# Kernel optimization log

Measured on AMD Instinct MI355X. Metric: run time of the kernel, lower is better.

Reference implementation:

```python
import jax, jax.numpy as jnp
import numpy as np

PAD = 2
STRIDE = 1

def _cayley(sig):
    # Geometric-product Cayley table G[i, j, k]: e_i * e_j = G[i, j, i^j] e_{i^j}
    # Blades indexed by bitmask over generators; sig = metric signature (+1/-1 per generator).
    n = len(sig)
    dim = 1 << n
    G = np.zeros((dim, dim, dim), dtype=np.float32)
    for a in range(dim):
        for b in range(dim):
            s = 0
            aa = a >> 1
            while aa:
                s += bin(aa & b).count('1')
                aa >>= 1
            sign = -1.0 if (s & 1) else 1.0
            common = a & b
            for i, m in enumerate(sig):
                if (common >> i) & 1:
                    sign *= m
            G[a, b, a ^ b] = sign
    return G


def setup_inputs() -> dict:
    key = jax.random.key(0)
    k1, k2, k3 = jax.random.split(key, 3)
    B, C, O, BD, L, K = 8, 64, 64, 8, 4096, 5
    x = jax.random.normal(k1, (B, C, BD, L), dtype=jnp.float32)
    bound = 1.0 / np.sqrt(C * BD * K)  # kaiming-style uniform bound
    W = jax.random.uniform(k2, (K, C, O, BD), minval=-bound, maxval=bound, dtype=jnp.float32)
    b = jax.random.uniform(k3, (1, O, BD, 1), minval=-bound, maxval=bound, dtype=jnp.float32)
    G = jnp.asarray(_cayley((1.0, 1.0, 1.0)))  # Cl(3,0), basis_dim = 8
    return {"x": x, "W": W, "b": b, "G": G}


def reference(x, W, b, G):
    # Original: pad length dim, unfold windows, then
    # result[b,o,k,w] = sum_{i,j,c,v} G[i,j,k] * W[v,c,o,i] * x_pad[b,c,j,w+v], plus bias.
    # Equivalent efficient form: pre-contract G with W into a conv kernel over
    # fused (channel, basis) axes and run a standard 1D convolution.
    K = W.shape[0]
    B, C, J, L = x.shape
    O = W.shape[2]
    Kb = G.shape[2]
    xp = jnp.pad(x, ((0, 0), (0, 0), (0, 0), (PAD, PAD)))  # padding_mode='zeros'
    # T[o,k,c,j,v] = sum_i G[i,j,k] W[v,c,o,i]  (tiny tensor: O*Kb x C*J x K)
    kern = jnp.einsum('ijk,vcoi->okcjv', G, W).reshape(O * Kb, C * J, K)
    xin = xp.reshape(B, C * J, L + 2 * PAD)
    out = jax.lax.conv_general_dilated(
        xin, kern, window_strides=(STRIDE,), padding='VALID',
        dimension_numbers=('NCH', 'OIH', 'NCH'))
    # out channels are (o major, k minor) per the reshape above
    return out.reshape(B, O, Kb, out.shape[-1]) + b
```

## Files before the change

### kernel.cpp

```cpp
#include <hip/hip_runtime.h>


#define C_    64
#define L_    4096
#define PAD_  2
#define OKch  512
#define KD_   2560

#define BM    128
#define BN    128
#define BKCJ  64
#define NCJB  8
#define NV    5
#define TILE  8192
#define ASTR  72
#define WIN   132

typedef __bf16 bf16x8 __attribute__((ext_vector_type(8)));
typedef float floatx4 __attribute__((ext_vector_type(4)));

__device__ __forceinline__ unsigned short f2bf(float f) {
    unsigned int u = __float_as_uint(f);
    u += 0x7FFFu + ((u >> 16) & 1u);
    return (unsigned short)(u >> 16);
}

#define WAIT_LGKM_0() asm volatile("s_waitcnt lgkmcnt(0)" ::: "memory")

__device__ __forceinline__ void barrier_raw() {
    asm volatile("" ::: "memory");
    __builtin_amdgcn_sched_barrier(0);
    __builtin_amdgcn_s_barrier();
    __builtin_amdgcn_sched_barrier(0);
    asm volatile("" ::: "memory");
}

__global__ __launch_bounds__(256) void build_kern(
    const float* __restrict__ W, const float* __restrict__ G,
    unsigned short* __restrict__ kernT)
{
    const int idx  = blockIdx.x * 256 + threadIdx.x;
    const int lrow = idx & 15;
    const int quad = (idx >> 4) & 3;
    const int f    = (idx >> 6) & 15;
    const int mq   = f >> 1;
    const int kk2  = f & 1;
    const int t    = idx >> 10;
    const int v    = t % 5;
    const int tc   = t / 5;
    const int cjb  = tc & 7;
    const int y    = tc >> 3;
    const int m    = (mq << 4) | lrow;
    const int ok   = (y << 7) | m;
    const int o    = ok >> 3;
    const int kb   = ok & 7;
    const int c    = (cjb << 3) | (kk2 << 2) | quad;

    const float* Wp = W + (((v * C_ + c) * 64 + o) << 3);
    const float4 w0 = *(const float4*)Wp;
    const float4 w1 = *(const float4*)(Wp + 4);
    const float w[8] = {w0.x, w0.y, w0.z, w0.w, w1.x, w1.y, w1.z, w1.w};

    unsigned int pk[4];
    #pragma unroll
    for (int j = 0; j < 8; j++) {
        float s = 0.f;
        #pragma unroll
        for (int i = 0; i < 8; i++)
            s += G[i * 64 + j * 8 + kb] * w[i];
        const unsigned short h = f2bf(s);
        if (j & 1) pk[j >> 1] |= (unsigned int)h << 16;
        else       pk[j >> 1]  = h;
    }
    uint4 uu; uu.x = pk[0]; uu.y = pk[1]; uu.z = pk[2]; uu.w = pk[3];
    *reinterpret_cast<uint4*>(
        &kernT[((size_t)t << 13) + (f << 9) + (quad << 7) + (lrow << 3)]) = uu;
}

__device__ __forceinline__ void b_issue(const float* xb, int cj0, int w0,
                                        float br[5][8]) {
    const int tid = threadIdx.x;
    #pragma unroll
    for (int u = 0; u < 5; u++) {
        int idx; bool act;
        if (u < 4) { idx = u * 256 + tid; act = true; }
        else { act = ((tid & 7) == 0);
               idx = 1024 + ((tid >> 6) << 3) + ((tid >> 3) & 7); }
        if (act) {
            const int kgrp = idx / WIN;
            const int nn   = idx - kgrp * WIN;
            int ws = w0 - PAD_ + nn;
            ws = ws < 0 ? 0 : (ws > (L_ - 1) ? (L_ - 1) : ws);
            const float* xp = xb + ((size_t)(cj0 + (kgrp << 3)) << 12) + (size_t)ws;
            #pragma unroll
            for (int r = 0; r < 8; r++)
                br[u][r] = xp[(size_t)r << 12];
        }
    }
}

__device__ __forceinline__ void b_store(unsigned short* BsP, const float br[5][8],
                                        int w0) {
    const int tid = threadIdx.x;
    #pragma unroll
    for (int u = 0; u < 5; u++) {
        int idx; bool act;
        if (u < 4) { idx = u * 256 + tid; act = true; }
        else { act = ((tid & 7) == 0);
               idx = 1024 + ((tid >> 6) << 3) + ((tid >> 3) & 7); }
        if (act) {
            const int kgrp = idx / WIN;
            const int nn   = idx - kgrp * WIN;
            const bool inb = (unsigned)(w0 - PAD_ + nn) < (unsigned)L_;
            unsigned int pk[4];
            #pragma unroll
            for (int r = 0; r < 8; r++) {
                const unsigned short h = f2bf(inb ? br[u][r] : 0.0f);
                if (r & 1) pk[r >> 1] |= (unsigned int)h << 16;
                else       pk[r >> 1]  = h;
            }
            uint4 uu; uu.x = pk[0]; uu.y = pk[1]; uu.z = pk[2]; uu.w = pk[3];
            *reinterpret_cast<uint4*>(&BsP[nn * ASTR + (kgrp << 3)]) = uu;
        }
    }
}

__device__ __forceinline__ void a_load(const unsigned short* t, int wb,
                                       bf16x8 r[8]) {
    #pragma unroll
    for (int f = 0; f < 8; f++)
        r[f] = *reinterpret_cast<const bf16x8*>(t + (f << 9) + wb);
}

__device__ __forceinline__ void compute_phase(
    const bf16x8 a[8], const unsigned short* BsP,
    int wn, int lrow, int quad, int v, floatx4 acc[4][4])
{
    #pragma unroll
    for (int kk2 = 0; kk2 < 2; kk2++) {
        bf16x8 bfr[4];
        #pragma unroll
        for (int nt = 0; nt < 4; nt++)
            bfr[nt] = *reinterpret_cast<const bf16x8*>(
                &BsP[(wn + (nt << 4) + lrow + v) * ASTR + (kk2 << 5) + (quad << 3)]);
        __builtin_amdgcn_s_setprio(1);
        #pragma unroll
        for (int mt = 0; mt < 4; mt++)
            #pragma unroll
            for (int nt = 0; nt < 4; nt++)
                acc[mt][nt] = __builtin_amdgcn_mfma_f32_16x16x32_bf16(
                    a[mt * 2 + kk2], bfr[nt], acc[mt][nt], 0, 0, 0);
        __builtin_amdgcn_s_setprio(0);
    }
}

__global__ __launch_bounds__(256, 2) void gpconv_mfma(
    const float* __restrict__ x, const unsigned short* __restrict__ kernT,
    const float* __restrict__ bias, float* __restrict__ out)
{
    __shared__ unsigned short Bs[WIN * ASTR];

    const int tid  = threadIdx.x;
    const int lane = tid & 63;
    const int wave = tid >> 6;
    const int lrow = lane & 15;
    const int quad = lane >> 4;
    const int wm = (wave >> 1) << 6;
    const int wn = (wave & 1) << 6;

    const int bid = blockIdx.x;
    const int y   = (bid >> 3) & 3;
    const int xw  = ((bid >> 5) << 3) + (bid & 7);
    const int b   = xw >> 5;
    const int w0  = (xw & 31) * BN;
    const int mBase = y * BM;
    const float* xb = x + (size_t)b * (size_t)(512 * L_);
    const unsigned short* ky = kernT + (size_t)(y * NCJB) * NV * TILE;

    const int wb = wm * 64 + lane * 8;

    floatx4 acc[4][4];
    {
        const floatx4 z = {0.f, 0.f, 0.f, 0.f};
        #pragma unroll
        for (int i2 = 0; i2 < 4; i2++)
            #pragma unroll
            for (int j2 = 0; j2 < 4; j2++) acc[i2][j2] = z;
    }

    bf16x8 aX[8], aY[8];
    float br[5][8];

    b_issue(xb, 0, w0, br);
    a_load(ky, wb, aX);
    b_store(Bs, br, w0);
    WAIT_LGKM_0();
    barrier_raw();

#define PHASE(CUR, NXT, CJB, V, DO_PRE, DO_BI, DO_ST)                        \
    {                                                                        \
        if (DO_PRE) a_load(ky + (size_t)((CJB) * 5 + (V) + 1) * TILE, wb, NXT); \
        if (DO_BI)  b_issue(xb, ((CJB) + 1) * BKCJ, w0, br);                 \
        compute_phase(CUR, Bs, wn, lrow, quad, (V), acc);                    \
        if (DO_ST) {                                                         \
            barrier_raw();                  \
            b_store(Bs, br, w0);       \
            WAIT_LGKM_0();                                                   \
            barrier_raw();                           \
        }                                                                    \
    }

    for (int cp = 0; cp < 3; cp++) {
        const int c0 = cp * 2, c1 = c0 + 1;
        PHASE(aX, aY, c0, 0, 1, 0, 0);
        PHASE(aY, aX, c0, 1, 1, 0, 0);
        PHASE(aX, aY, c0, 2, 1, 0, 0);
        PHASE(aY, aX, c0, 3, 1, 1, 0);
        PHASE(aX, aY, c0, 4, 1, 0, 1);
        PHASE(aY, aX, c1, 0, 1, 0, 0);
        PHASE(aX, aY, c1, 1, 1, 0, 0);
        PHASE(aY, aX, c1, 2, 1, 0, 0);
        PHASE(aX, aY, c1, 3, 1, 1, 0);
        PHASE(aY, aX, c1, 4, 1, 0, 1);
    }
    PHASE(aX, aY, 6, 0, 1, 0, 0);
    PHASE(aY, aX, 6, 1, 1, 0, 0);
    PHASE(aX, aY, 6, 2, 1, 0, 0);
    PHASE(aY, aX, 6, 3, 1, 1, 0);
    PHASE(aX, aY, 6, 4, 1, 0, 1);
    PHASE(aY, aX, 7, 0, 1, 0, 0);
    PHASE(aX, aY, 7, 1, 1, 0, 0);
    PHASE(aY, aX, 7, 2, 1, 0, 0);
    PHASE(aX, aY, 7, 3, 1, 0, 0);
    PHASE(aY, aX, 7, 4, 0, 0, 0);
#undef PHASE

    #pragma unroll
    for (int mt = 0; mt < 4; mt++) {
        #pragma unroll
        for (int e = 0; e < 4; e++) {
            const int okc = mBase + wm + (mt << 4) + (quad << 2) + e;
            const float bv = bias[okc];
            float* orow = out + ((size_t)b * OKch + (size_t)okc) * L_ + w0;
            #pragma unroll
            for (int nt = 0; nt < 4; nt++) {
                const int n = wn + (nt << 4) + lrow;
                orow[n] = acc[mt][nt][e] + bv;
            }
        }
    }
}

extern "C" void kernel_launch(void* const* d_in, const int* in_sizes, int n_in,
                              void* d_out, int out_size, void* d_ws, size_t ws_size,
                              hipStream_t stream) {
    const float* x    = (const float*)d_in[0];
    const float* W    = (const float*)d_in[1];
    const float* bias = (const float*)d_in[2];
    const float* G    = (const float*)d_in[3];
    unsigned short* kernT = (unsigned short*)d_ws;
    float* out = (float*)d_out;

    build_kern<<<dim3(640), 256, 0, stream>>>(W, G, kernT);
    gpconv_mfma<<<dim3(1024), 256, 0, stream>>>(x, kernT, bias, out);
}
```

Baseline: 184.9 us.

## Double-buffer x tile in LDS with XOR swizzle and split staged loads

```diff
diff --git a/kernel.cpp b/kernel.cpp
--- a/kernel.cpp
+++ b/kernel.cpp
@@ -13,8 +13,8 @@
 #define NCJB  8
 #define NV    5
 #define TILE  8192
-#define ASTR  72
 #define WIN   132
+#define BSZ   (WIN * 64)
 
 typedef __bf16 bf16x8 __attribute__((ext_vector_type(8)));
 typedef float floatx4 __attribute__((ext_vector_type(4)));
@@ -77,51 +77,73 @@
         &kernT[((size_t)t << 13) + (f << 9) + (quad << 7) + (lrow << 3)]) = uu;
 }
 
-__device__ __forceinline__ void b_issue(const float* xb, int cj0, int w0,
-                                        float br[5][8]) {
-    const int tid = threadIdx.x;
-    #pragma unroll
-    for (int u = 0; u < 5; u++) {
-        int idx; bool act;
-        if (u < 4) { idx = u * 256 + tid; act = true; }
-        else { act = ((tid & 7) == 0);
-               idx = 1024 + ((tid >> 6) << 3) + ((tid >> 3) & 7); }
-        if (act) {
-            const int kgrp = idx / WIN;
-            const int nn   = idx - kgrp * WIN;
-            int ws = w0 - PAD_ + nn;
-            ws = ws < 0 ? 0 : (ws > (L_ - 1) ? (L_ - 1) : ws);
-            const float* xp = xb + ((size_t)(cj0 + (kgrp << 3)) << 12) + (size_t)ws;
-            #pragma unroll
-            for (int r = 0; r < 8; r++)
-                br[u][r] = xp[(size_t)r << 12];
-        }
-    }
-}
-
-__device__ __forceinline__ void b_store(unsigned short* BsP, const float br[5][8],
+__device__ __forceinline__ void bi_half(const float* xb, int cj0, int w0,
+                                        int base, float br[2][8]) {
+    const int tid = threadIdx.x;
+    #pragma unroll
+    for (int u = 0; u < 2; u++) {
+        const int idx  = base + u * 256 + tid;
+        const int kgrp = idx / WIN;
+        const int nn   = idx - kgrp * WIN;
+        int ws = w0 - PAD_ + nn;
+        ws = ws < 0 ? 0 : (ws > (L_ - 1) ? (L_ - 1) : ws);
+        const float* xp = xb + ((size_t)(cj0 + (kgrp << 3)) << 12) + (size_t)ws;
+        #pragma unroll
+        for (int r = 0; r < 8; r++)
+            br[u][r] = xp[(size_t)r << 12];
+    }
+}
+
+__device__ __forceinline__ void bi_tail(const float* xb, int cj0, int w0,
+                                        float brT[8]) {
+    const int tid = threadIdx.x;
+    if ((tid & 7) == 0) {
+        const int idx  = 1024 + ((tid >> 6) << 3) + ((tid >> 3) & 7);
+        const int kgrp = idx / WIN;
+        const int nn   = idx - kgrp * WIN;
+        int ws = w0 - PAD_ + nn;
+        ws = ws < 0 ? 0 : (ws > (L_ - 1) ? (L_ - 1) : ws);
+        const float* xp = xb + ((size_t)(cj0 + (kgrp << 3)) << 12) + (size_t)ws;
+        #pragma unroll
+        for (int r = 0; r < 8; r++)
+            brT[r] = xp[(size_t)r << 12];
+    }
+}
+
+__device__ __forceinline__ void st_item(unsigned short* Bw, int kgrp, int nn,
+                                        int w0, const float br[8]) {
+    const bool inb = (unsigned)(w0 - PAD_ + nn) < (unsigned)L_;
+    unsigned int pk[4];
+    #pragma unroll
+    for (int r = 0; r < 8; r++) {
+        const unsigned short h = f2bf(inb ? br[r] : 0.0f);
+        if (r & 1) pk[r >> 1] |= (unsigned int)h << 16;
+        else       pk[r >> 1]  = h;
+    }
+    uint4 uu; uu.x = pk[0]; uu.y = pk[1]; uu.z = pk[2]; uu.w = pk[3];
+    *reinterpret_cast<uint4*>(&Bw[(nn << 6) + ((kgrp ^ (nn & 7)) << 3)]) = uu;
+}
+
+__device__ __forceinline__ void st_half(unsigned short* Bw, int base,
+                                        const float br[2][8], int w0) {
+    const int tid = threadIdx.x;
+    #pragma unroll
+    for (int u = 0; u < 2; u++) {
+        const int idx  = base + u * 256 + tid;
+        const int kgrp = idx / WIN;
+        const int nn   = idx - kgrp * WIN;
+        st_item(Bw, kgrp, nn, w0, br[u]);
+    }
+}
+
+__device__ __forceinline__ void st_tail(unsigned short* Bw, const float brT[8],
                                         int w0) {
     const int tid = threadIdx.x;
-    #pragma unroll
-    for (int u = 0; u < 5; u++) {
-        int idx; bool act;
-        if (u < 4) { idx = u * 256 + tid; act = true; }
-        else { act = ((tid & 7) == 0);
-               idx = 1024 + ((tid >> 6) << 3) + ((tid >> 3) & 7); }
-        if (act) {
-            const int kgrp = idx / WIN;
-            const int nn   = idx - kgrp * WIN;
-            const bool inb = (unsigned)(w0 - PAD_ + nn) < (unsigned)L_;
-            unsigned int pk[4];
-            #pragma unroll
-            for (int r = 0; r < 8; r++) {
-                const unsigned short h = f2bf(inb ? br[u][r] : 0.0f);
-                if (r & 1) pk[r >> 1] |= (unsigned int)h << 16;
-                else       pk[r >> 1]  = h;
-            }
-            uint4 uu; uu.x = pk[0]; uu.y = pk[1]; uu.z = pk[2]; uu.w = pk[3];
-            *reinterpret_cast<uint4*>(&BsP[nn * ASTR + (kgrp << 3)]) = uu;
-        }
+    if ((tid & 7) == 0) {
+        const int idx  = 1024 + ((tid >> 6) << 3) + ((tid >> 3) & 7);
+        const int kgrp = idx / WIN;
+        const int nn   = idx - kgrp * WIN;
+        st_item(Bw, kgrp, nn, w0, brT);
     }
 }
 
@@ -133,16 +155,19 @@
 }
 
 __device__ __forceinline__ void compute_phase(
-    const bf16x8 a[8], const unsigned short* BsP,
+    const bf16x8 a[8], const unsigned short* BsR,
     int wn, int lrow, int quad, int v, floatx4 acc[4][4])
 {
+    const int s7  = (lrow + v) & 7;
+    const int rb0 = (wn + lrow + v) << 6;
     #pragma unroll
     for (int kk2 = 0; kk2 < 2; kk2++) {
+        const int col = (((kk2 << 2) | quad) ^ s7) << 3;
         bf16x8 bfr[4];
         #pragma unroll
         for (int nt = 0; nt < 4; nt++)
             bfr[nt] = *reinterpret_cast<const bf16x8*>(
-                &BsP[(wn + (nt << 4) + lrow + v) * ASTR + (kk2 << 5) + (quad << 3)]);
+                &BsR[rb0 + (nt << 10) + col]);
         __builtin_amdgcn_s_setprio(1);
         #pragma unroll
         for (int mt = 0; mt < 4; mt++)
@@ -154,11 +179,11 @@
     }
 }
 
-__global__ __launch_bounds__(256, 2) void gpconv_mfma(
+__global__ __launch_bounds__(256, 3) void gpconv_mfma(
     const float* __restrict__ x, const unsigned short* __restrict__ kernT,
     const float* __restrict__ bias, float* __restrict__ out)
 {
-    __shared__ unsigned short Bs[WIN * ASTR];
+    __shared__ unsigned short Bs[2 * BSZ];
 
     const int tid  = threadIdx.x;
     const int lane = tid & 63;
@@ -189,50 +214,56 @@
     }
 
     bf16x8 aX[8], aY[8];
-    float br[5][8];
-
-    b_issue(xb, 0, w0, br);
+    float brA[2][8], brB[2][8], brT[8];
+
+    bi_half(xb, 0, w0, 0, brA);
+    bi_half(xb, 0, w0, 512, brB);
+    bi_tail(xb, 0, w0, brT);
     a_load(ky, wb, aX);
-    b_store(Bs, br, w0);
+    st_half(Bs, 0, brA, w0);
+    st_half(Bs, 512, brB, w0);
+    st_tail(Bs, brT, w0);
     WAIT_LGKM_0();
     barrier_raw();
 
-#define PHASE(CUR, NXT, CJB, V, DO_PRE, DO_BI, DO_ST)                        \
-    {                                                                        \
-        if (DO_PRE) a_load(ky + (size_t)((CJB) * 5 + (V) + 1) * TILE, wb, NXT); \
-        if (DO_BI)  b_issue(xb, ((CJB) + 1) * BKCJ, w0, br);                 \
-        compute_phase(CUR, Bs, wn, lrow, quad, (V), acc);                    \
-        if (DO_ST) {                                                         \
-            barrier_raw();                  \
-            b_store(Bs, br, w0);       \
-            WAIT_LGKM_0();                                                   \
-            barrier_raw();                           \
-        }                                                                    \
+#define PHASE(CUR, NXT, CJB, V, STG, LASTP)                                   \
+    {                                                                         \
+        const unsigned short* BsR = Bs + (((CJB) & 1) ? BSZ : 0);             \
+        unsigned short*       BsW = Bs + (((CJB) & 1) ? 0 : BSZ);             \
+        if ((STG) && (V) == 3) st_half(BsW, 0, brA, w0);                      \
+        if ((STG) && (V) == 4) { st_half(BsW, 512, brB, w0);                  \
+                                 st_tail(BsW, brT, w0); }                     \
+        if (!(LASTP)) a_load(ky + (size_t)((CJB) * 5 + (V) + 1) * TILE, wb, NXT); \
+        if ((STG) && (V) == 2) bi_half(xb, ((CJB) + 1) * BKCJ, w0, 0, brA);   \
+        if ((STG) && (V) == 3) { bi_half(xb, ((CJB) + 1) * BKCJ, w0, 512, brB); \
+                                 bi_tail(xb, ((CJB) + 1) * BKCJ, w0, brT); }  \
+        compute_phase(CUR, BsR, wn, lrow, quad, (V), acc);                    \
+        if ((STG) && (V) == 4) { WAIT_LGKM_0(); barrier_raw(); }              \
     }
 
     for (int cp = 0; cp < 3; cp++) {
         const int c0 = cp * 2, c1 = c0 + 1;
-        PHASE(aX, aY, c0, 0, 1, 0, 0);
-        PHASE(aY, aX, c0, 1, 1, 0, 0);
-        PHASE(aX, aY, c0, 2, 1, 0, 0);
-        PHASE(aY, aX, c0, 3, 1, 1, 0);
-        PHASE(aX, aY, c0, 4, 1, 0, 1);
-        PHASE(aY, aX, c1, 0, 1, 0, 0);
-        PHASE(aX, aY, c1, 1, 1, 0, 0);
-        PHASE(aY, aX, c1, 2, 1, 0, 0);
-        PHASE(aX, aY, c1, 3, 1, 1, 0);
-        PHASE(aY, aX, c1, 4, 1, 0, 1);
-    }
-    PHASE(aX, aY, 6, 0, 1, 0, 0);
-    PHASE(aY, aX, 6, 1, 1, 0, 0);
-    PHASE(aX, aY, 6, 2, 1, 0, 0);
-    PHASE(aY, aX, 6, 3, 1, 1, 0);
-    PHASE(aX, aY, 6, 4, 1, 0, 1);
-    PHASE(aY, aX, 7, 0, 1, 0, 0);
-    PHASE(aX, aY, 7, 1, 1, 0, 0);
-    PHASE(aY, aX, 7, 2, 1, 0, 0);
-    PHASE(aX, aY, 7, 3, 1, 0, 0);
-    PHASE(aY, aX, 7, 4, 0, 0, 0);
+        PHASE(aX, aY, c0, 0, 1, 0);
+        PHASE(aY, aX, c0, 1, 1, 0);
+        PHASE(aX, aY, c0, 2, 1, 0);
+        PHASE(aY, aX, c0, 3, 1, 0);
+        PHASE(aX, aY, c0, 4, 1, 0);
+        PHASE(aY, aX, c1, 0, 1, 0);
+        PHASE(aX, aY, c1, 1, 1, 0);
+        PHASE(aY, aX, c1, 2, 1, 0);
+        PHASE(aX, aY, c1, 3, 1, 0);
+        PHASE(aY, aX, c1, 4, 1, 0);
+    }
+    PHASE(aX, aY, 6, 0, 1, 0);
+    PHASE(aY, aX, 6, 1, 1, 0);
+    PHASE(aX, aY, 6, 2, 1, 0);
+    PHASE(aY, aX, 6, 3, 1, 0);
+    PHASE(aX, aY, 6, 4, 1, 0);
+    PHASE(aY, aX, 7, 0, 0, 0);
+    PHASE(aX, aY, 7, 1, 0, 0);
+    PHASE(aY, aX, 7, 2, 0, 0);
+    PHASE(aX, aY, 7, 3, 0, 0);
+    PHASE(aY, aX, 7, 4, 0, 1);
 #undef PHASE
 
     #pragma unroll
```

After: 425.7 us. +130.2%, slower.

## Pre-pad x to bf16, double-buffer LDS with swizzle, pipeline loads via inline asm

Applied to the files above, without the earlier changes.

```diff
diff --git a/kernel.cpp b/kernel.cpp
--- a/kernel.cpp
+++ b/kernel.cpp
@@ -5,7 +5,7 @@
 #define L_    4096
 #define PAD_  2
 #define OKch  512
-#define KD_   2560
+#define XSTR  4104
 
 #define BM    128
 #define BN    128
@@ -13,8 +13,8 @@
 #define NCJB  8
 #define NV    5
 #define TILE  8192
-#define ASTR  72
 #define WIN   132
+#define BSZ   (WIN * 64)
 
 typedef __bf16 bf16x8 __attribute__((ext_vector_type(8)));
 typedef float floatx4 __attribute__((ext_vector_type(4)));
@@ -26,6 +26,8 @@
 }
 
 #define WAIT_LGKM_0() asm volatile("s_waitcnt lgkmcnt(0)" ::: "memory")
+#define WAITV_(N) asm volatile("s_waitcnt vmcnt(" #N ")" ::: "memory")
+#define WAITV(N) do { WAITV_(N); __builtin_amdgcn_sched_barrier(0); } while (0)
 
 __device__ __forceinline__ void barrier_raw() {
     asm volatile("" ::: "memory");
@@ -35,138 +37,192 @@
     asm volatile("" ::: "memory");
 }
 
-__global__ __launch_bounds__(256) void build_kern(
+#define GLD_U32(dst, ptr) \
+    asm volatile("global_load_dword %0, %1, off" : "=&v"(dst) : "v"(ptr))
+#define GLD_A4(a0, a1, a2, a3, ptr)                          \
+    asm volatile("global_load_dwordx4 %0, %4, off\n\t"       \
+                 "global_load_dwordx4 %1, %4, off offset:1024\n\t" \
+                 "global_load_dwordx4 %2, %4, off offset:2048\n\t" \
+                 "global_load_dwordx4 %3, %4, off offset:3072"     \
+                 : "=&v"(a0), "=&v"(a1), "=&v"(a2), "=&v"(a3) : "v"(ptr))
+
+__global__ __launch_bounds__(256) void prep(
     const float* __restrict__ W, const float* __restrict__ G,
-    unsigned short* __restrict__ kernT)
+    const float* __restrict__ x,
+    unsigned short* __restrict__ kernT, unsigned short* __restrict__ xp)
 {
-    const int idx  = blockIdx.x * 256 + threadIdx.x;
-    const int lrow = idx & 15;
-    const int quad = (idx >> 4) & 3;
-    const int f    = (idx >> 6) & 15;
-    const int mq   = f >> 1;
-    const int kk2  = f & 1;
-    const int t    = idx >> 10;
-    const int v    = t % 5;
-    const int tc   = t / 5;
-    const int cjb  = tc & 7;
-    const int y    = tc >> 3;
-    const int m    = (mq << 4) | lrow;
-    const int ok   = (y << 7) | m;
-    const int o    = ok >> 3;
-    const int kb   = ok & 7;
-    const int c    = (cjb << 3) | (kk2 << 2) | quad;
-
-    const float* Wp = W + (((v * C_ + c) * 64 + o) << 3);
-    const float4 w0 = *(const float4*)Wp;
-    const float4 w1 = *(const float4*)(Wp + 4);
-    const float w[8] = {w0.x, w0.y, w0.z, w0.w, w1.x, w1.y, w1.z, w1.w};
-
-    unsigned int pk[4];
+    const int bid = blockIdx.x;
+    const int tid = threadIdx.x;
+    if (bid < 640) {
+        __shared__ float Gs[512];
+        Gs[tid] = G[tid];
+        Gs[tid + 256] = G[tid + 256];
+        __syncthreads();
+
+        const int idx  = bid * 256 + tid;
+        const int lrow = idx & 15;
+        const int quad = (idx >> 4) & 3;
+        const int f    = (idx >> 6) & 15;
+        const int mq   = f >> 1;
+        const int kk2  = f & 1;
+        const int t    = idx >> 10;
+        const int v    = t % 5;
+        const int tc   = t / 5;
+        const int cjb  = tc & 7;
+        const int y    = tc >> 3;
+        const int m    = (mq << 4) | lrow;
+        const int ok   = (y << 7) | m;
+        const int o    = ok >> 3;
+        const int kb   = ok & 7;
+        const int c    = (cjb << 3) | (kk2 << 2) | quad;
+
+        const float* Wp = W + (((v * C_ + c) * 64 + o) << 3);
+        const float4 w0 = *(const float4*)Wp;
+        const float4 w1 = *(const float4*)(Wp + 4);
+        const float w[8] = {w0.x, w0.y, w0.z, w0.w, w1.x, w1.y, w1.z, w1.w};
+
+        unsigned int pk[4];
+        #pragma unroll
+        for (int j = 0; j < 8; j++) {
+            float s = 0.f;
+            #pragma unroll
+            for (int i = 0; i < 8; i++)
+                s += Gs[i * 64 + j * 8 + kb] * w[i];
+            const unsigned short h = f2bf(s);
+            if (j & 1) pk[j >> 1] |= (unsigned int)h << 16;
+            else       pk[j >> 1]  = h;
+        }
+        uint4 uu; uu.x = pk[0]; uu.y = pk[1]; uu.z = pk[2]; uu.w = pk[3];
+        *reinterpret_cast<uint4*>(
+            &kernT[((size_t)t << 13) + (f << 9) + (quad << 7) + (lrow << 3)]) = uu;
+    } else {
+        const int row = bid - 640;
+        const float* src = x + (size_t)row * L_;
+        unsigned short* dst = xp + (size_t)row * XSTR;
+        #pragma unroll
+        for (int i = 0; i < 4; i++) {
+            const int p = (i * 256 + tid) << 2;
+            const float4 fv = *reinterpret_cast<const float4*>(src + p);
+            const unsigned int u0 = (unsigned int)f2bf(fv.x) | ((unsigned int)f2bf(fv.y) << 16);
+            const unsigned int u1 = (unsigned int)f2bf(fv.z) | ((unsigned int)f2bf(fv.w) << 16);
+            *reinterpret_cast<unsigned int*>(dst + 2 + p) = u0;
+            *reinterpret_cast<unsigned int*>(dst + 4 + p) = u1;
+        }
+        if (tid == 0) {
+            *reinterpret_cast<unsigned int*>(dst) = 0u;
+            *reinterpret_cast<unsigned int*>(dst + 4098) = 0u;
+        }
+    }
+}
+
+__device__ __forceinline__ void bi_round(const unsigned short* xp, int cj0,
+                                         int w0, int round, unsigned int (&d)[8]) {
+    const int idx  = round * 256 + (int)threadIdx.x;
+    const int kgrp = idx / 66;
+    const int wp   = idx - kgrp * 66;
+    const unsigned short* p =
+        xp + (size_t)(cj0 + (kgrp << 3)) * XSTR + (size_t)(w0 + (wp << 1));
+    GLD_U32(d[0], p);
+    GLD_U32(d[1], p + XSTR);
+    GLD_U32(d[2], p + 2 * XSTR);
+    GLD_U32(d[3], p + 3 * XSTR);
+    GLD_U32(d[4], p + 4 * XSTR);
+    GLD_U32(d[5], p + 5 * XSTR);
+    GLD_U32(d[6], p + 6 * XSTR);
+    GLD_U32(d[7], p + 7 * XSTR);
+}
+
+__device__ __forceinline__ void bi_tail(const unsigned short* xp, int cj0,
+                                        int w0, unsigned int (&d)[8]) {
+    const int lane = (int)threadIdx.x & 63;
+    const int wave = (int)threadIdx.x >> 6;
+    if ((lane & 15) == 0) {
+        const int idx  = 512 + (wave << 2) + (lane >> 4);
+        const int kgrp = idx / 66;
+        const int wp   = idx - kgrp * 66;
+        const unsigned short* p =
+            xp + (size_t)(cj0 + (kgrp << 3)) * XSTR + (size_t)(w0 + (wp << 1));
+        GLD_U32(d[0], p);
+        GLD_U32(d[1], p + XSTR);
+        GLD_U32(d[2], p + 2 * XSTR);
+        GLD_U32(d[3], p + 3 * XSTR);
+        GLD_U32(d[4], p + 4 * XSTR);
+        GLD_U32(d[5], p + 5 * XSTR);
+        GLD_U32(d[6], p + 6 * XSTR);
+        GLD_U32(d[7], p + 7 * XSTR);
+    }
+}
+
+__device__ __forceinline__ void st_item(unsigned short* Bw, int kgrp, int nn,
+                                        const unsigned int (&d)[8]) {
+    const unsigned int lo0 = (d[0] & 0xffffu) | (d[1] << 16);
+    const unsigned int hi0 = (d[0] >> 16)     | (d[1] & 0xffff0000u);
+    const unsigned int lo1 = (d[2] & 0xffffu) | (d[3] << 16);
+    const unsigned int hi1 = (d[2] >> 16)     | (d[3] & 0xffff0000u);
+    const unsigned int lo2 = (d[4] & 0xffffu) | (d[5] << 16);
+    const unsigned int hi2 = (d[4] >> 16)     | (d[5] & 0xffff0000u);
+    const unsigned int lo3 = (d[6] & 0xffffu) | (d[7] << 16);
+    const unsigned int hi3 = (d[6] >> 16)     | (d[7] & 0xffff0000u);
+    const int s = kgrp ^ (nn & 7);
+    uint4 Lv; Lv.x = lo0; Lv.y = lo1; Lv.z = lo2; Lv.w = lo3;
+    uint4 Hv; Hv.x = hi0; Hv.y = hi1; Hv.z = hi2; Hv.w = hi3;
+    *reinterpret_cast<uint4*>(&Bw[(nn << 6) + (s << 3)]) = Lv;
+    *reinterpret_cast<uint4*>(&Bw[((nn + 1) << 6) + ((s ^ 1) << 3)]) = Hv;
+}
+
+__device__ __forceinline__ void st_round(unsigned short* Bw, int round,
+                                         const unsigned int (&d)[8]) {
+    const int idx  = round * 256 + (int)threadIdx.x;
+    const int kgrp = idx / 66;
+    const int wp   = idx - kgrp * 66;
+    st_item(Bw, kgrp, wp << 1, d);
+}
+
+__device__ __forceinline__ void st_tail(unsigned short* Bw,
+                                        const unsigned int (&d)[8]) {
+    const int lane = (int)threadIdx.x & 63;
+    const int wave = (int)threadIdx.x >> 6;
+    if ((lane & 15) == 0) {
+        const int idx  = 512 + (wave << 2) + (lane >> 4);
+        const int kgrp = idx / 66;
+        const int wp   = idx - kgrp * 66;
+        st_item(Bw, kgrp, wp << 1, d);
+    }
+}
+
+__device__ __forceinline__ void bfread(const unsigned short* BsR, int v, int kk2,
+                                       int lrow, int quad, bf16x8 (&f)[8]) {
+    const int s7  = (lrow + v) & 7;
+    const int col = ((((kk2) << 2) | quad) ^ s7) << 3;
+    const int rb  = (lrow + v) << 6;
     #pragma unroll
-    for (int j = 0; j < 8; j++) {
-        float s = 0.f;
-        #pragma unroll
-        for (int i = 0; i < 8; i++)
-            s += G[i * 64 + j * 8 + kb] * w[i];
-        const unsigned short h = f2bf(s);
-        if (j & 1) pk[j >> 1] |= (unsigned int)h << 16;
-        else       pk[j >> 1]  = h;
-    }
-    uint4 uu; uu.x = pk[0]; uu.y = pk[1]; uu.z = pk[2]; uu.w = pk[3];
-    *reinterpret_cast<uint4*>(
-        &kernT[((size_t)t << 13) + (f << 9) + (quad << 7) + (lrow << 3)]) = uu;
-}
-
-__device__ __forceinline__ void b_issue(const float* xb, int cj0, int w0,
-                                        float br[5][8]) {
-    const int tid = threadIdx.x;
+    for (int nt = 0; nt < 8; nt++)
+        f[nt] = *reinterpret_cast<const bf16x8*>(&BsR[rb + (nt << 10) + col]);
+}
+
+__device__ __forceinline__ void cl(const bf16x8 (&a)[4], int kk2,
+                                   const bf16x8 (&f)[8], floatx4 (&acc)[2][8]) {
+    __builtin_amdgcn_s_setprio(1);
     #pragma unroll
-    for (int u = 0; u < 5; u++) {
-        int idx; bool act;
-        if (u < 4) { idx = u * 256 + tid; act = true; }
-        else { act = ((tid & 7) == 0);
-               idx = 1024 + ((tid >> 6) << 3) + ((tid >> 3) & 7); }
-        if (act) {
-            const int kgrp = idx / WIN;
-            const int nn   = idx - kgrp * WIN;
-            int ws = w0 - PAD_ + nn;
-            ws = ws < 0 ? 0 : (ws > (L_ - 1) ? (L_ - 1) : ws);
-            const float* xp = xb + ((size_t)(cj0 + (kgrp << 3)) << 12) + (size_t)ws;
-            #pragma unroll
-            for (int r = 0; r < 8; r++)
-                br[u][r] = xp[(size_t)r << 12];
-        }
-    }
-}
-
-__device__ __forceinline__ void b_store(unsigned short* BsP, const float br[5][8],
-                                        int w0) {
-    const int tid = threadIdx.x;
-    #pragma unroll
-    for (int u = 0; u < 5; u++) {
-        int idx; bool act;
-        if (u < 4) { idx = u * 256 + tid; act = true; }
-        else { act = ((tid & 7) == 0);
-               idx = 1024 + ((tid >> 6) << 3) + ((tid >> 3) & 7); }
-        if (act) {
-            const int kgrp = idx / WIN;
-            const int nn   = idx - kgrp * WIN;
-            const bool inb = (unsigned)(w0 - PAD_ + nn) < (unsigned)L_;
-            unsigned int pk[4];
-            #pragma unroll
-            for (int r = 0; r < 8; r++) {
-                const unsigned short h = f2bf(inb ? br[u][r] : 0.0f);
-                if (r & 1) pk[r >> 1] |= (unsigned int)h << 16;
-                else       pk[r >> 1]  = h;
-            }
-            uint4 uu; uu.x = pk[0]; uu.y = pk[1]; uu.z = pk[2]; uu.w = pk[3];
-            *reinterpret_cast<uint4*>(&BsP[nn * ASTR + (kgrp << 3)]) = uu;
-        }
-    }
-}
-
-__device__ __forceinline__ void a_load(const unsigned short* t, int wb,
-                                       bf16x8 r[8]) {
-    #pragma unroll
-    for (int f = 0; f < 8; f++)
-        r[f] = *reinterpret_cast<const bf16x8*>(t + (f << 9) + wb);
-}
-
-__device__ __forceinline__ void compute_phase(
-    const bf16x8 a[8], const unsigned short* BsP,
-    int wn, int lrow, int quad, int v, floatx4 acc[4][4])
-{
-    #pragma unroll
-    for (int kk2 = 0; kk2 < 2; kk2++) {
-        bf16x8 bfr[4];
-        #pragma unroll
-        for (int nt = 0; nt < 4; nt++)
-            bfr[nt] = *reinterpret_cast<const bf16x8*>(
-                &BsP[(wn + (nt << 4) + lrow + v) * ASTR + (kk2 << 5) + (quad << 3)]);
-        __builtin_amdgcn_s_setprio(1);
-        #pragma unroll
-        for (int mt = 0; mt < 4; mt++)
-            #pragma unroll
-            for (int nt = 0; nt < 4; nt++)
-                acc[mt][nt] = __builtin_amdgcn_mfma_f32_16x16x32_bf16(
-                    a[mt * 2 + kk2], bfr[nt], acc[mt][nt], 0, 0, 0);
-        __builtin_amdgcn_s_setprio(0);
-    }
+    for (int mt = 0; mt < 2; mt++)
+        #pragma unroll
+        for (int nt = 0; nt < 8; nt++)
+            acc[mt][nt] = __builtin_amdgcn_mfma_f32_16x16x32_bf16(
+                a[mt * 2 + kk2], f[nt], acc[mt][nt], 0, 0, 0);
+    __builtin_amdgcn_s_setprio(0);
 }
 
 __global__ __launch_bounds__(256, 2) void gpconv_mfma(
-    const float* __restrict__ x, const unsigned short* __restrict__ kernT,
+    const unsigned short* __restrict__ xp, const unsigned short* __restrict__ kernT,
     const float* __restrict__ bias, float* __restrict__ out)
 {
-    __shared__ unsigned short Bs[WIN * ASTR];
+    __shared__ unsigned short Bs[2 * BSZ];
 
     const int tid  = threadIdx.x;
     const int lane = tid & 63;
     const int wave = tid >> 6;
     const int lrow = lane & 15;
     const int quad = lane >> 4;
-    const int wm = (wave >> 1) << 6;
-    const int wn = (wave & 1) << 6;
 
     const int bid = blockIdx.x;
     const int y   = (bid >> 3) & 3;
@@ -174,77 +230,89 @@
     const int b   = xw >> 5;
     const int w0  = (xw & 31) * BN;
     const int mBase = y * BM;
-    const float* xb = x + (size_t)b * (size_t)(512 * L_);
+    const unsigned short* xb = xp + (size_t)b * (size_t)(512 * XSTR);
     const unsigned short* ky = kernT + (size_t)(y * NCJB) * NV * TILE;
-
-    const int wb = wm * 64 + lane * 8;
-
-    floatx4 acc[4][4];
+    const unsigned short* abase = ky + (wave << 11) + (lane << 3);
+
+    floatx4 acc[2][8];
     {
         const floatx4 z = {0.f, 0.f, 0.f, 0.f};
         #pragma unroll
-        for (int i2 = 0; i2 < 4; i2++)
+        for (int i2 = 0; i2 < 2; i2++)
             #pragma unroll
-            for (int j2 = 0; j2 < 4; j2++) acc[i2][j2] = z;
-    }
-
-    bf16x8 aX[8], aY[8];
-    float br[5][8];
-
-    b_issue(xb, 0, w0, br);
-    a_load(ky, wb, aX);
-    b_store(Bs, br, w0);
+            for (int j2 = 0; j2 < 8; j2++) acc[i2][j2] = z;
+    }
+
+    bf16x8 aX[4], aY[4];
+    unsigned int dA[8], dB[8], dT[8];
+
+    bi_round(xb, 0, w0, 0, dA);
+    bi_round(xb, 0, w0, 1, dB);
+    bi_tail(xb, 0, w0, dT);
+    GLD_A4(aX[0], aX[1], aX[2], aX[3], abase);
+    WAITV(4);
+    st_round(Bs, 0, dA);
+    st_round(Bs, 1, dB);
+    st_tail(Bs, dT);
     WAIT_LGKM_0();
     barrier_raw();
 
-#define PHASE(CUR, NXT, CJB, V, DO_PRE, DO_BI, DO_ST)                        \
-    {                                                                        \
-        if (DO_PRE) a_load(ky + (size_t)((CJB) * 5 + (V) + 1) * TILE, wb, NXT); \
-        if (DO_BI)  b_issue(xb, ((CJB) + 1) * BKCJ, w0, br);                 \
-        compute_phase(CUR, Bs, wn, lrow, quad, (V), acc);                    \
-        if (DO_ST) {                                                         \
-            barrier_raw();                  \
-            b_store(Bs, br, w0);       \
-            WAIT_LGKM_0();                                                   \
-            barrier_raw();                           \
-        }                                                                    \
+#define PHASE(CUR, NXT, CJB, V, STG, LASTP, WCMP)                             \
+    {                                                                         \
+        const unsigned short* BsR = Bs + (((CJB) & 1) ? BSZ : 0);             \
+        unsigned short*       BsW = Bs + (((CJB) & 1) ? 0 : BSZ);             \
+        if ((STG) && (V) == 3) { WAITV(4); st_round(BsW, 0, dA); }            \
+        if ((STG) && (V) == 4) { WAITV(4); st_round(BsW, 1, dB);              \
+                                 st_tail(BsW, dT); }                          \
+        bf16x8 f0[8], f1[8];                                                  \
+        bfread(BsR, (V), 0, lrow, quad, f0);                                  \
+        if ((STG) && (V) == 2) bi_round(xb, ((CJB) + 1) * BKCJ, w0, 0, dA);   \
+        if ((STG) && (V) == 3) { bi_round(xb, ((CJB) + 1) * BKCJ, w0, 1, dB); \
+                                 bi_tail(xb, ((CJB) + 1) * BKCJ, w0, dT); }   \
+        if (!(LASTP)) GLD_A4(NXT[0], NXT[1], NXT[2], NXT[3],                  \
+                             abase + (size_t)((CJB) * 5 + (V) + 1) * TILE);   \
+        WAITV(WCMP);                                                          \
+        cl(CUR, 0, f0, acc);                                                  \
+        bfread(BsR, (V), 1, lrow, quad, f1);                                  \
+        cl(CUR, 1, f1, acc);                                                  \
+        if ((STG) && (V) == 4) { WAIT_LGKM_0(); barrier_raw(); }              \
     }
 
     for (int cp = 0; cp < 3; cp++) {
         const int c0 = cp * 2, c1 = c0 + 1;
-        PHASE(aX, aY, c0, 0, 1, 0, 0);
-        PHASE(aY, aX, c0, 1, 1, 0, 0);
-        PHASE(aX, aY, c0, 2, 1, 0, 0);
-        PHASE(aY, aX, c0, 3, 1, 1, 0);
-        PHASE(aX, aY, c0, 4, 1, 0, 1);
-        PHASE(aY, aX, c1, 0, 1, 0, 0);
-        PHASE(aX, aY, c1, 1, 1, 0, 0);
-        PHASE(aY, aX, c1, 2, 1, 0, 0);
-        PHASE(aX, aY, c1, 3, 1, 1, 0);
-        PHASE(aY, aX, c1, 4, 1, 0, 1);
-    }
-    PHASE(aX, aY, 6, 0, 1, 0, 0);
-    PHASE(aY, aX, 6, 1, 1, 0, 0);
-    PHASE(aX, aY, 6, 2, 1, 0, 0);
-    PHASE(aY, aX, 6, 3, 1, 1, 0);
-    PHASE(aX, aY, 6, 4, 1, 0, 1);
-    PHASE(aY, aX, 7, 0, 1, 0, 0);
-    PHASE(aX, aY, 7, 1, 1, 0, 0);
-    PHASE(aY, aX, 7, 2, 1, 0, 0);
-    PHASE(aX, aY, 7, 3, 1, 0, 0);
-    PHASE(aY, aX, 7, 4, 0, 0, 0);
+        PHASE(aX, aY, c0, 0, 1, 0, 4);
+        PHASE(aY, aX, c0, 1, 1, 0, 4);
+        PHASE(aX, aY, c0, 2, 1, 0, 12);
+        PHASE(aY, aX, c0, 3, 1, 0, 20);
+        PHASE(aX, aY, c0, 4, 1, 0, 4);
+        PHASE(aY, aX, c1, 0, 1, 0, 4);
+        PHASE(aX, aY, c1, 1, 1, 0, 4);
+        PHASE(aY, aX, c1, 2, 1, 0, 12);
+        PHASE(aX, aY, c1, 3, 1, 0, 20);
+        PHASE(aY, aX, c1, 4, 1, 0, 4);
+    }
+    PHASE(aX, aY, 6, 0, 1, 0, 4);
+    PHASE(aY, aX, 6, 1, 1, 0, 4);
+    PHASE(aX, aY, 6, 2, 1, 0, 12);
+    PHASE(aY, aX, 6, 3, 1, 0, 20);
+    PHASE(aX, aY, 6, 4, 1, 0, 4);
+    PHASE(aY, aX, 7, 0, 0, 0, 4);
+    PHASE(aX, aY, 7, 1, 0, 0, 4);
+    PHASE(aY, aX, 7, 2, 0, 0, 4);
+    PHASE(aX, aY, 7, 3, 0, 0, 4);
+    PHASE(aY, aX, 7, 4, 0, 1, 0);
 #undef PHASE
 
     #pragma unroll
-    for (int mt = 0; mt < 4; mt++) {
+    for (int mt = 0; mt < 2; mt++) {
         #pragma unroll
         for (int e = 0; e < 4; e++) {
-            const int okc = mBase + wm + (mt << 4) + (quad << 2) + e;
+            const int okc = mBase + (wave << 5) + (mt << 4) + (quad << 2) + e;
             const float bv = bias[okc];
             float* orow = out + ((size_t)b * OKch + (size_t)okc) * L_ + w0;
             #pragma unroll
-            for (int nt = 0; nt < 4; nt++) {
-                const int n = wn + (nt << 4) + lrow;
+            for (int nt = 0; nt < 8; nt++) {
+                const int n = (nt << 4) + lrow;
                 orow[n] = acc[mt][nt][e] + bv;
             }
         }
@@ -259,8 +327,9 @@
     const float* bias = (const float*)d_in[2];
     const float* G    = (const float*)d_in[3];
     unsigned short* kernT = (unsigned short*)d_ws;
+    unsigned short* xp    = (unsigned short*)((char*)d_ws + (4 << 20));
     float* out = (float*)d_out;
 
-    build_kern<<<dim3(640), 256, 0, stream>>>(W, G, kernT);
-    gpconv_mfma<<<dim3(1024), 256, 0, stream>>>(x, kernT, bias, out);
-}
+    prep<<<dim3(640 + 4096), 256, 0, stream>>>(W, G, x, kernT, xp);
+    gpconv_mfma<<<dim3(1024), 256, 0, stream>>>(xp, kernT, bias, out);
+}
```

Result: faster. 178.3 us (-3.6%).
